# Optimization experiments

Measured on AMD Instinct MI355X. Metric: run time of the kernel, lower is better.

## Reference

```python
import jax, jax.numpy as jnp
import numpy as np

ANCHOR = 12.0      # anchor (d,h,w) size used for parametrization
NMS_IOU = 0.25     # suppression threshold
TOPK = 2048        # pre-NMS candidate cap (= stop_after), fixed for jit


def setup_inputs() -> dict:
    key = jax.random.key(0)
    k1, k2 = jax.random.split(key)
    bboxes = jax.random.normal(k1, (2, 6, 64, 96, 96), dtype=jnp.float32)
    scores = jax.random.normal(k2, (2, 64, 96, 96), dtype=jnp.float32)
    return {"bboxes": bboxes, "scores": scores}


def _deparametrize(bboxes):
    # bboxes: (B, 6, D, H, W), parametrized as in Ren et al. 2017
    D, H, W = bboxes.shape[2:]
    axes = [jnp.arange(s, dtype=bboxes.dtype) + 0.5 for s in (D, H, W)]
    zyx = jnp.stack(jnp.meshgrid(*axes, indexing='ij'))        # (3, D, H, W)
    abs_zyx = bboxes[:, :3] * ANCHOR + zyx[None]               # center coords
    abs_dhw = jnp.exp(bboxes[:, 3:]) * ANCHOR                  # sizes
    return jnp.concatenate([abs_zyx, abs_dhw], axis=1)


def _pairwise_iou(b1, b2):
    # b1: (N,6), b2: (M,6) with (z,y,x,d,h,w)
    c1, s1 = b1[:, :3], b1[:, 3:]
    c2, s2 = b2[:, :3], b2[:, 3:]
    lo = jnp.maximum((c1 - s1 / 2)[:, None, :], (c2 - s2 / 2)[None, :, :])
    hi = jnp.minimum((c1 + s1 / 2)[:, None, :], (c2 + s2 / 2)[None, :, :])
    inter = jnp.clip(hi - lo, 0).prod(-1)                      # (N, M)
    union = s1.prod(-1)[:, None] + s2.prod(-1)[None, :] - inter
    return inter / union


def _nms_one(boxes_flat, scores_flat):
    # boxes_flat: (P, 6), scores_flat: (P,)
    scores_top, idx = jax.lax.top_k(scores_flat, TOPK)
    boxes_top = boxes_flat[idx]                                # (K, 6)
    ious = _pairwise_iou(boxes_top, boxes_top)                 # (K, K)
    ar = jnp.arange(TOPK)

    def body(keep, i):
        # suppress lower-scored boxes overlapping a kept box i
        suppress = (ious[i] > NMS_IOU) & (ar > i) & keep[i]
        return keep & ~suppress, None

    keep, _ = jax.lax.scan(body, jnp.ones(TOPK, dtype=bool), ar)
    out = jnp.concatenate([scores_top[:, None], boxes_top], axis=1)  # (K, 7)
    return jnp.where(keep[:, None], out, 0.0)


def reference(bboxes, scores):
    abs_boxes = _deparametrize(bboxes)                         # (B, 6, D, H, W)
    B = bboxes.shape[0]
    boxes_flat = abs_boxes.reshape(B, 6, -1).transpose(0, 2, 1)  # (B, P, 6)
    scores_flat = scores.reshape(B, -1)                          # (B, P)
    # (B, TOPK, 7): column 0 = score, columns 1:7 = (z,y,x,d,h,w); suppressed rows zeroed
    return jax.vmap(_nms_one)(boxes_flat, scores_flat)
```

## Files before the change

kernel.cpp:

```cpp
#include <hip/hip_runtime.h>
#include <math.h>

typedef unsigned int U32;
typedef unsigned long long U64;

constexpr int N_SP   = 64 * 96 * 96;
constexpr int NBATCH = 2;
constexpr int K_TOP  = 2048;
constexpr int NBINS  = 8192;
constexpr int CAP    = 8192;
constexpr float ANCHOR_F = 12.0f;
constexpr float NMS_IOU_F = 0.25f;

constexpr size_t OFF_HIST = 0;
constexpr size_t OFF_CNT  = OFF_HIST + 2 * NBINS * 4;
constexpr size_t OFF_THR  = OFF_CNT + 256;
constexpr size_t OFF_RANK = OFF_THR + 256;
constexpr size_t OFF_CAND = OFF_RANK + 2 * CAP * 4;
constexpr size_t OFF_BOX  = OFF_CAND + 2 * CAP * 8;
constexpr size_t OFF_MASK = OFF_BOX + 2 * 14 * K_TOP * 4;

__device__ __forceinline__ U32 mono_of(float f) {
  U32 u = __float_as_uint(f);
  return (u & 0x80000000u) ? ~u : (u | 0x80000000u);
}
__device__ __forceinline__ float un_mono(U32 m) {
  U32 u = (m & 0x80000000u) ? (m ^ 0x80000000u) : ~m;
  return __uint_as_float(u);
}

__global__ void __launch_bounds__(256) k_zero(U32* hist, U32* rank, U32* cnt) {
  int g = blockIdx.x * 256 + threadIdx.x;
  hist[g] = 0;
  rank[g] = 0;
  if (g < NBATCH) cnt[g] = 0;
}

__global__ void __launch_bounds__(256) k_hist(const float* __restrict__ scores,
                                              U32* __restrict__ hist) {
  int b = blockIdx.y;
  const float4* s4 = (const float4*)(scores + (size_t)b * N_SP)
                     + (size_t)blockIdx.x * 2048 + threadIdx.x;
  float4 v[8];
#pragma unroll
  for (int e = 0; e < 8; ++e) v[e] = s4[e * 256];
  __shared__ U32 lh[NBINS];
  for (int k = threadIdx.x; k < NBINS; k += 256) lh[k] = 0;
  __syncthreads();
#pragma unroll
  for (int e = 0; e < 8; ++e) {
    atomicAdd(&lh[mono_of(v[e].x) >> 19], 1u);
    atomicAdd(&lh[mono_of(v[e].y) >> 19], 1u);
    atomicAdd(&lh[mono_of(v[e].z) >> 19], 1u);
    atomicAdd(&lh[mono_of(v[e].w) >> 19], 1u);
  }
  __syncthreads();
  U32* gh = hist + (size_t)b * NBINS;
  for (int k = threadIdx.x; k < NBINS; k += 256) {
    U32 c = lh[k];
    if (c) atomicAdd(&gh[k], c);
  }
}

__global__ void __launch_bounds__(256) k_thresh(const U32* __restrict__ hist,
                                                U32* __restrict__ thr) {
  int b = blockIdx.x;
  const U32* h = hist + (size_t)b * NBINS;
  __shared__ U32 part[256];
  int t = threadIdx.x;
  int base = NBINS - 32 * (t + 1);
  U32 s = 0;
  for (int k = 0; k < 32; ++k) s += h[base + k];
  part[t] = s;
  __syncthreads();
  if (t == 0) {
    U32 cum = 0, bin = 0;
    for (int c = 0; c < 256; ++c) {
      U32 p = part[c];
      if (cum + p >= (U32)K_TOP) {
        int hb = NBINS - 32 * c - 1;
        for (int k = 0; k < 32; ++k) {
          cum += h[hb - k];
          if (cum >= (U32)K_TOP) { bin = (U32)(hb - k); break; }
        }
        break;
      }
      cum += p;
    }
    thr[b] = bin;
  }
}

__global__ void __launch_bounds__(256) k_collect(const float* __restrict__ scores,
                                                 const U32* __restrict__ thr,
                                                 U32* __restrict__ cnt,
                                                 U64* __restrict__ cand) {
  int b = blockIdx.y;
  U32 tb = thr[b];
  const float4* s4 = (const float4*)(scores + (size_t)b * N_SP)
                     + (size_t)blockIdx.x * 1024 + threadIdx.x;
  float4 v[4];
#pragma unroll
  for (int e = 0; e < 4; ++e) v[e] = s4[e * 256];
  __shared__ U64 lbuf[4096];
  __shared__ U32 lcnt, lbase;
  if (threadIdx.x == 0) lcnt = 0;
  __syncthreads();
#pragma unroll
  for (int e = 0; e < 4; ++e) {
    U32 i0 = (blockIdx.x * 1024 + e * 256 + threadIdx.x) * 4;
    float vv[4] = {v[e].x, v[e].y, v[e].z, v[e].w};
#pragma unroll
    for (int c = 0; c < 4; ++c) {
      U32 m = mono_of(vv[c]);
      if ((m >> 19) >= tb) {
        U32 p = atomicAdd(&lcnt, 1u);
        lbuf[p] = ((U64)m << 32) | (U32)(~(i0 + c));
      }
    }
  }
  __syncthreads();
  if (threadIdx.x == 0 && lcnt) lbase = atomicAdd(&cnt[b], lcnt);
  __syncthreads();
  U32 n = lcnt;
  if (n == 0) return;
  U32 base = lbase;
  U64* cb = cand + (size_t)b * CAP;
  for (U32 k = threadIdx.x; k < n; k += 256) {
    U32 pos = base + k;
    if (pos < (U32)CAP) cb[pos] = lbuf[k];
  }
}

__global__ void __launch_bounds__(256) k_count(const U64* __restrict__ cand,
                                               const U32* __restrict__ cnt,
                                               U32* __restrict__ rank) {
  int b = blockIdx.y;
  U32 C = cnt[b]; if (C > (U32)CAP) C = CAP;
  U32 g = blockIdx.x * 256 + threadIdx.x;
  U32 t = g & (CAP - 1);
  U32 sgm = g >> 13;
  if (t >= C) return;
  const U64* cb = cand + (size_t)b * CAP;
  U64 key = cb[t];
  U32 segLen = (C + 7) >> 3;
  U32 j0 = sgm * segLen;
  U32 j1 = j0 + segLen; if (j1 > C) j1 = C;
  U32 c = 0;
  for (U32 j = j0; j < j1; ++j) c += (cb[j] > key) ? 1u : 0u;
  if (c) atomicAdd(&rank[(size_t)b * CAP + t], c);
}

#pragma clang fp contract(off)

__global__ void __launch_bounds__(256) k_gather(const float* __restrict__ bboxes,
                                                const U64* __restrict__ cand,
                                                const U32* __restrict__ cnt,
                                                const U32* __restrict__ rank,
                                                float* __restrict__ box) {
  int b = blockIdx.y;
  U32 C = cnt[b]; if (C > (U32)CAP) C = CAP;
  U32 t = blockIdx.x * 256 + threadIdx.x;
  if (t >= C) return;
  U32 r = rank[(size_t)b * CAP + t];
  if (r >= (U32)K_TOP) return;
  U64 key = cand[(size_t)b * CAP + t];
  U32 idx = ~(U32)(key & 0xFFFFFFFFull);
  float sc = un_mono((U32)(key >> 32));
  int d = idx / 9216;
  int rem = idx - d * 9216;
  int h = rem / 96;
  int w = rem - h * 96;
  const float* src = bboxes + (size_t)b * 6 * N_SP + idx;
  float r0 = src[0];
  float r1 = src[(size_t)N_SP];
  float r2 = src[(size_t)2 * N_SP];
  float r3 = src[(size_t)3 * N_SP];
  float r4 = src[(size_t)4 * N_SP];
  float r5 = src[(size_t)5 * N_SP];
  float cz = r0 * ANCHOR_F + ((float)d + 0.5f);
  float cy = r1 * ANCHOR_F + ((float)h + 0.5f);
  float cx = r2 * ANCHOR_F + ((float)w + 0.5f);
  float sz = (float)exp((double)r3) * ANCHOR_F;
  float sy = (float)exp((double)r4) * ANCHOR_F;
  float sx = (float)exp((double)r5) * ANCHOR_F;
  float* B0 = box + (size_t)b * 14 * K_TOP;
  B0[0 * K_TOP + r] = cz;  B0[1 * K_TOP + r] = cy;  B0[2 * K_TOP + r] = cx;
  B0[3 * K_TOP + r] = sz;  B0[4 * K_TOP + r] = sy;  B0[5 * K_TOP + r] = sx;
  B0[6 * K_TOP + r] = cz - sz * 0.5f;
  B0[7 * K_TOP + r] = cy - sy * 0.5f;
  B0[8 * K_TOP + r] = cx - sx * 0.5f;
  B0[9 * K_TOP + r] = cz + sz * 0.5f;
  B0[10 * K_TOP + r] = cy + sy * 0.5f;
  B0[11 * K_TOP + r] = cx + sx * 0.5f;
  B0[12 * K_TOP + r] = (sz * sy) * sx;
  B0[13 * K_TOP + r] = sc;
}

__global__ void __launch_bounds__(256) k_mask(const float* __restrict__ box,
                                              U32* __restrict__ mask) {
  int b = blockIdx.y;
  int it = blockIdx.x >> 2;
  int jq = blockIdx.x & 3;
  const float* B0 = box + (size_t)b * 14 * K_TOP;
  __shared__ float ls[7][512];
  int j0 = jq * 512;
  for (int k = threadIdx.x; k < 7 * 512; k += 256) {
    int a = k >> 9, j = k & 511;
    ls[a][j] = B0[(size_t)(6 + a) * K_TOP + j0 + j];
  }
  __syncthreads();
  int lane = threadIdx.x & 63;
  int wv = threadIdx.x >> 6;
  int i = it * 64 + lane;
  float imin0 = B0[6 * K_TOP + i], imin1 = B0[7 * K_TOP + i], imin2 = B0[8 * K_TOP + i];
  float imax0 = B0[9 * K_TOP + i], imax1 = B0[10 * K_TOP + i], imax2 = B0[11 * K_TOP + i];
  float ivol  = B0[12 * K_TOP + i];
  U32 wbits[4];
  int jb = wv * 128;
#pragma unroll
  for (int wl = 0; wl < 4; ++wl) {
    U32 bits = 0;
    for (int bit = 0; bit < 32; ++bit) {
      int jl = jb + wl * 32 + bit;
      int j = j0 + jl;
      float lo0 = fmaxf(imin0, ls[0][jl]);
      float lo1 = fmaxf(imin1, ls[1][jl]);
      float lo2 = fmaxf(imin2, ls[2][jl]);
      float hi0 = fminf(imax0, ls[3][jl]);
      float hi1 = fminf(imax1, ls[4][jl]);
      float hi2 = fminf(imax2, ls[5][jl]);
      float d0 = fmaxf(hi0 - lo0, 0.0f);
      float d1 = fmaxf(hi1 - lo1, 0.0f);
      float d2 = fmaxf(hi2 - lo2, 0.0f);
      float inter = (d0 * d1) * d2;
      float uni = (ivol + ls[6][jl]) - inter;
      float iou = inter / uni;
      bits |= ((iou > NMS_IOU_F) && (j > i)) ? (1u << bit) : 0u;
    }
    wbits[wl] = bits;
  }
  uint4* mrow = (uint4*)(mask + ((size_t)(b * K_TOP + i)) * 64);
  mrow[jq * 4 + wv] = make_uint4(wbits[0], wbits[1], wbits[2], wbits[3]);
}

__global__ void __launch_bounds__(256) k_nms(const float* __restrict__ box,
                                             const U32* __restrict__ mask,
                                             float* __restrict__ out) {
  int b = blockIdx.x;
  int tid = threadIdx.x;
  int wv = tid >> 6, lane = tid & 63;
  const U32* mk = mask + (size_t)b * K_TOP * 64;
  __shared__ U32 sbuf[8][64 * 64];
  __shared__ U32 keepArr[64];

#define STAGE(cc)                                                              \
  do {                                                                         \
    U32* dst = sbuf[(cc) & 7];                                                 \
    const U32* gsrc = mk + (size_t)(cc) * 4096;                                \
    _Pragma("unroll") for (int k = 0; k < 8; ++k) {                            \
      int ins = (wv - 1) * 8 + k;                                              \
      __builtin_amdgcn_global_load_lds(                                        \
          (const __attribute__((address_space(1))) U32*)(gsrc + ins * 256 +    \
                                                         lane * 4),            \
          (__attribute__((address_space(3))) U32*)(dst + ins * 256), 16, 0, 0);\
    }                                                                          \
  } while (0)

  if (wv == 1 || wv == 2) {
    for (int cc = 0; cc < 6; ++cc) STAGE(cc);
    asm volatile("s_waitcnt vmcnt(40)" ::: "memory");
  }
  __builtin_amdgcn_s_barrier();
  asm volatile("" ::: "memory");

  U32 keep = 0xFFFFFFFFu;
  for (int c = 0; c < 32; ++c) {
    if (wv == 0) {
      const U32* base = sbuf[c & 7];
      for (int blk = 0; blk < 2; ++blk) {
        int g = c * 2 + blk;
        U32 rw[32];
#pragma unroll
        for (int q = 0; q < 32; ++q) rw[q] = base[(blk * 32 + q) * 64 + lane];
        U32 kw = (U32)__builtin_amdgcn_readlane((int)keep, g);
        U32 dg[32];
#pragma unroll
        for (int q = 0; q < 32; ++q)
          dg[q] = (U32)__builtin_amdgcn_readlane((int)rw[q], g);
#pragma unroll
        for (int q = 0; q < 32; ++q)
          kw = (kw & (1u << q)) ? (kw & ~dg[q]) : kw;
        U32 acc = 0;
#pragma unroll
        for (int q = 0; q < 32; ++q) {
          U32 sel = (kw & (1u << q)) ? 0xFFFFFFFFu : 0u;
          acc |= sel & rw[q];
        }
        keep &= ~acc;
      }
    } else if (wv <= 2) {
      if (c + 6 < 32) {
        STAGE(c + 6);
        asm volatile("s_waitcnt vmcnt(40)" ::: "memory");
      } else if (c == 26) { asm volatile("s_waitcnt vmcnt(32)" ::: "memory");
      } else if (c == 27) { asm volatile("s_waitcnt vmcnt(24)" ::: "memory");
      } else if (c == 28) { asm volatile("s_waitcnt vmcnt(16)" ::: "memory");
      } else if (c == 29) { asm volatile("s_waitcnt vmcnt(8)"  ::: "memory");
      } else              { asm volatile("s_waitcnt vmcnt(0)"  ::: "memory");
      }
    }
    __builtin_amdgcn_s_barrier();
    asm volatile("" ::: "memory");
  }
#undef STAGE

  if (wv == 0) keepArr[lane] = keep;
  __syncthreads();

  const float* B0 = box + (size_t)b * 14 * K_TOP;
  for (int t = tid; t < K_TOP; t += 256) {
    U32 kp = (keepArr[t >> 5] >> (t & 31)) & 1u;
    float sc = B0[13 * K_TOP + t];
    float vz = B0[0 * K_TOP + t], vy = B0[1 * K_TOP + t], vx = B0[2 * K_TOP + t];
    float dz = B0[3 * K_TOP + t], dy = B0[4 * K_TOP + t], dx = B0[5 * K_TOP + t];
    float* o = out + (size_t)(b * K_TOP + t) * 7;
    o[0] = kp ? sc : 0.0f;
    o[1] = kp ? vz : 0.0f;
    o[2] = kp ? vy : 0.0f;
    o[3] = kp ? vx : 0.0f;
    o[4] = kp ? dz : 0.0f;
    o[5] = kp ? dy : 0.0f;
    o[6] = kp ? dx : 0.0f;
  }
}

extern "C" void kernel_launch(void* const* d_in, const int* in_sizes, int n_in,
                              void* d_out, int out_size, void* d_ws, size_t ws_size,
                              hipStream_t stream) {
  const float* bboxes = (const float*)d_in[0];
  const float* scores = (const float*)d_in[1];
  float* out = (float*)d_out;

  char* ws = (char*)d_ws;
  U32* hist = (U32*)(ws + OFF_HIST);
  U32* cnt  = (U32*)(ws + OFF_CNT);
  U32* thr  = (U32*)(ws + OFF_THR);
  U32* rank = (U32*)(ws + OFF_RANK);
  U64* cand = (U64*)(ws + OFF_CAND);
  float* box = (float*)(ws + OFF_BOX);
  U32* mask = (U32*)(ws + OFF_MASK);

  k_zero<<<64, 256, 0, stream>>>(hist, rank, cnt);
  k_hist<<<dim3(72, NBATCH), 256, 0, stream>>>(scores, hist);
  k_thresh<<<NBATCH, 256, 0, stream>>>(hist, thr);
  k_collect<<<dim3(144, NBATCH), 256, 0, stream>>>(scores, thr, cnt, cand);
  k_count<<<dim3(256, NBATCH), 256, 0, stream>>>(cand, cnt, rank);
  k_gather<<<dim3(CAP / 256, NBATCH), 256, 0, stream>>>(bboxes, cand, cnt, rank, box);
  k_mask<<<dim3(128, NBATCH), 256, 0, stream>>>(box, mask);
  k_nms<<<NBATCH, 256, 0, stream>>>(box, mask, out);
}
```

Baseline: 198.3 us.

## Precompute diagonal mask words and make NMS scan sparse over kept boxes

k_mask now also writes each box's diagonal-block suppression word to a separate diag array. k_nms preloads those words into registers up front instead of reading 32 LDS rows and doing readlanes for every block. It then walks only the still-kept bits with ctz loops, skipping fully suppressed blocks, and ORs in only the mask rows of kept boxes. This trades the fixed unrolled per-block work for data-dependent loops with a software-pipelined LDS load, and wave 3 now only takes part in the barriers.

```diff
diff --git a/kernel.cpp b/kernel.cpp
--- a/kernel.cpp
+++ b/kernel.cpp
@@ -19,6 +19,7 @@
 constexpr size_t OFF_CAND = OFF_RANK + 2 * CAP * 4;
 constexpr size_t OFF_BOX  = OFF_CAND + 2 * CAP * 8;
 constexpr size_t OFF_MASK = OFF_BOX + 2 * 14 * K_TOP * 4;
+constexpr size_t OFF_DIAG = OFF_MASK + 2 * K_TOP * 64 * 4;
 
 __device__ __forceinline__ U32 mono_of(float f) {
   U32 u = __float_as_uint(f);
@@ -198,7 +199,8 @@
 }
 
 __global__ void __launch_bounds__(256) k_mask(const float* __restrict__ box,
-                                              U32* __restrict__ mask) {
+                                              U32* __restrict__ mask,
+                                              U32* __restrict__ diag) {
   int b = blockIdx.y;
   int it = blockIdx.x >> 2;
   int jq = blockIdx.x & 3;
@@ -242,15 +244,23 @@
   }
   uint4* mrow = (uint4*)(mask + ((size_t)(b * K_TOP + i)) * 64);
   mrow[jq * 4 + wv] = make_uint4(wbits[0], wbits[1], wbits[2], wbits[3]);
+  U32* dgp = diag + (size_t)b * K_TOP;
+#pragma unroll
+  for (int wl = 0; wl < 4; ++wl) {
+    int w = jq * 16 + wv * 4 + wl;
+    if (w == (i >> 5)) dgp[i] = wbits[wl];
+  }
 }
 
 __global__ void __launch_bounds__(256) k_nms(const float* __restrict__ box,
                                              const U32* __restrict__ mask,
+                                             const U32* __restrict__ diag,
                                              float* __restrict__ out) {
   int b = blockIdx.x;
   int tid = threadIdx.x;
   int wv = tid >> 6, lane = tid & 63;
   const U32* mk = mask + (size_t)b * K_TOP * 64;
+  const U32* dgp = diag + (size_t)b * K_TOP;
   __shared__ U32 sbuf[8][64 * 64];
   __shared__ U32 keepArr[64];
 
@@ -267,39 +277,14 @@
     }                                                                          \
   } while (0)
 
+  U32 keep = 0xFFFFFFFFu;
+
   if (wv == 1 || wv == 2) {
     for (int cc = 0; cc < 6; ++cc) STAGE(cc);
     asm volatile("s_waitcnt vmcnt(40)" ::: "memory");
-  }
-  __builtin_amdgcn_s_barrier();
-  asm volatile("" ::: "memory");
-
-  U32 keep = 0xFFFFFFFFu;
-  for (int c = 0; c < 32; ++c) {
-    if (wv == 0) {
-      const U32* base = sbuf[c & 7];
-      for (int blk = 0; blk < 2; ++blk) {
-        int g = c * 2 + blk;
-        U32 rw[32];
-#pragma unroll
-        for (int q = 0; q < 32; ++q) rw[q] = base[(blk * 32 + q) * 64 + lane];
-        U32 kw = (U32)__builtin_amdgcn_readlane((int)keep, g);
-        U32 dg[32];
-#pragma unroll
-        for (int q = 0; q < 32; ++q)
-          dg[q] = (U32)__builtin_amdgcn_readlane((int)rw[q], g);
-#pragma unroll
-        for (int q = 0; q < 32; ++q)
-          kw = (kw & (1u << q)) ? (kw & ~dg[q]) : kw;
-        U32 acc = 0;
-#pragma unroll
-        for (int q = 0; q < 32; ++q) {
-          U32 sel = (kw & (1u << q)) ? 0xFFFFFFFFu : 0u;
-          acc |= sel & rw[q];
-        }
-        keep &= ~acc;
-      }
-    } else if (wv <= 2) {
+    __builtin_amdgcn_s_barrier();
+    asm volatile("" ::: "memory");
+    for (int c = 0; c < 32; ++c) {
       if (c + 6 < 32) {
         STAGE(c + 6);
         asm volatile("s_waitcnt vmcnt(40)" ::: "memory");
@@ -309,13 +294,74 @@
       } else if (c == 29) { asm volatile("s_waitcnt vmcnt(8)"  ::: "memory");
       } else              { asm volatile("s_waitcnt vmcnt(0)"  ::: "memory");
       }
-    }
+      __builtin_amdgcn_s_barrier();
+      asm volatile("" ::: "memory");
+    }
+  } else if (wv == 3) {
+    __builtin_amdgcn_s_barrier();
+    for (int c = 0; c < 32; ++c) __builtin_amdgcn_s_barrier();
+  } else {
+#define DLOAD(K) U32 dW##K = dgp[(K) * 64 + lane];
+    DLOAD(0)  DLOAD(1)  DLOAD(2)  DLOAD(3)  DLOAD(4)  DLOAD(5)  DLOAD(6)  DLOAD(7)
+    DLOAD(8)  DLOAD(9)  DLOAD(10) DLOAD(11) DLOAD(12) DLOAD(13) DLOAD(14) DLOAD(15)
+    DLOAD(16) DLOAD(17) DLOAD(18) DLOAD(19) DLOAD(20) DLOAD(21) DLOAD(22) DLOAD(23)
+    DLOAD(24) DLOAD(25) DLOAD(26) DLOAD(27) DLOAD(28) DLOAD(29) DLOAD(30) DLOAD(31)
+#undef DLOAD
     __builtin_amdgcn_s_barrier();
     asm volatile("" ::: "memory");
+
+#define BLOCKR(CC, BLK, DREG)                                                  \
+    {                                                                          \
+      int g = (CC) * 2 + (BLK);                                                \
+      U32 kw = (U32)__builtin_amdgcn_readlane((int)keep, g);                   \
+      if (kw) {                                                                \
+        U32 m = kw;                                                            \
+        while (m) {                      \
+          int q = __builtin_ctz(m);                                            \
+          U32 d = (U32)__builtin_amdgcn_readlane((int)DREG, (BLK) * 32 + q);   \
+          kw &= ~d;        \
+          m &= ~d;                                                             \
+          m &= m - 1;          \
+        }                                                                      \
+        U32 acc = 0;                                                           \
+        U32 m2 = kw;                        \
+        if (m2) {                                                              \
+          int q0 = __builtin_ctz(m2); m2 &= m2 - 1;                            \
+          U32 r0 = base[((BLK) * 32 + q0) * 64 + lane];                        \
+          while (m2) {                           \
+            int q1 = __builtin_ctz(m2); m2 &= m2 - 1;                          \
+            U32 r1 = base[((BLK) * 32 + q1) * 64 + lane];                      \
+            acc |= r0;                                                         \
+            r0 = r1;                                                           \
+          }                                                                    \
+          acc |= r0;                                                           \
+        }                                                                      \
+        keep &= ~acc;            \
+      }                                                                        \
+    }
+
+#define CHUNK(CC, DREG)                                                        \
+    {                                                                          \
+      const U32* base = &sbuf[(CC) & 7][0];                                    \
+      BLOCKR(CC, 0, DREG)                                                      \
+      BLOCKR(CC, 1, DREG)                                                      \
+      __builtin_amdgcn_s_barrier();                                            \
+      asm volatile("" ::: "memory");                                           \
+    }
+
+    CHUNK(0, dW0)   CHUNK(1, dW1)   CHUNK(2, dW2)   CHUNK(3, dW3)
+    CHUNK(4, dW4)   CHUNK(5, dW5)   CHUNK(6, dW6)   CHUNK(7, dW7)
+    CHUNK(8, dW8)   CHUNK(9, dW9)   CHUNK(10, dW10) CHUNK(11, dW11)
+    CHUNK(12, dW12) CHUNK(13, dW13) CHUNK(14, dW14) CHUNK(15, dW15)
+    CHUNK(16, dW16) CHUNK(17, dW17) CHUNK(18, dW18) CHUNK(19, dW19)
+    CHUNK(20, dW20) CHUNK(21, dW21) CHUNK(22, dW22) CHUNK(23, dW23)
+    CHUNK(24, dW24) CHUNK(25, dW25) CHUNK(26, dW26) CHUNK(27, dW27)
+    CHUNK(28, dW28) CHUNK(29, dW29) CHUNK(30, dW30) CHUNK(31, dW31)
+#undef CHUNK
+#undef BLOCKR
+    keepArr[lane] = keep;
   }
 #undef STAGE
-
-  if (wv == 0) keepArr[lane] = keep;
   __syncthreads();
 
   const float* B0 = box + (size_t)b * 14 * K_TOP;
@@ -350,6 +396,7 @@
   U64* cand = (U64*)(ws + OFF_CAND);
   float* box = (float*)(ws + OFF_BOX);
   U32* mask = (U32*)(ws + OFF_MASK);
+  U32* diag = (U32*)(ws + OFF_DIAG);
 
   k_zero<<<64, 256, 0, stream>>>(hist, rank, cnt);
   k_hist<<<dim3(72, NBATCH), 256, 0, stream>>>(scores, hist);
@@ -357,6 +404,6 @@
   k_collect<<<dim3(144, NBATCH), 256, 0, stream>>>(scores, thr, cnt, cand);
   k_count<<<dim3(256, NBATCH), 256, 0, stream>>>(cand, cnt, rank);
   k_gather<<<dim3(CAP / 256, NBATCH), 256, 0, stream>>>(bboxes, cand, cnt, rank, box);
-  k_mask<<<dim3(128, NBATCH), 256, 0, stream>>>(box, mask);
-  k_nms<<<NBATCH, 256, 0, stream>>>(box, mask, out);
-}
+  k_mask<<<dim3(128, NBATCH), 256, 0, stream>>>(box, mask, diag);
+  k_nms<<<NBATCH, 256, 0, stream>>>(box, mask, diag, out);
+}
```

Result: slower. 271.7 us (+37.0%).
